# Kernel optimization log

Hardware: AMD Instinct MI355X
Metric: run time of the kernel (lower is better)

The kernel has to match this reference:

```python
import jax, jax.numpy as jnp
import numpy as np

B, N, C = 128, 196, 2048   # batch, regions (14x14), conv channels
H, A = 512, 512            # hidden_size, attention_size


def setup_inputs() -> dict:
    key = jax.random.key(0)
    ks = jax.random.split(key, 10)
    s = lambda d: 1.0 / np.sqrt(d)
    return {
        "img_embedding": jax.random.normal(ks[0], (B, N, C), jnp.float32),
        "hidden": jax.random.normal(ks[1], (B, H), jnp.float32),
        "W_img": jax.random.uniform(ks[2], (C, A), jnp.float32, -s(C), s(C)),
        "b_img": jax.random.uniform(ks[3], (A,), jnp.float32, -s(C), s(C)),
        "W_hid": jax.random.uniform(ks[4], (H, A), jnp.float32, -s(H), s(H)),
        "b_hid": jax.random.uniform(ks[5], (A,), jnp.float32, -s(H), s(H)),
        "w_att": jax.random.uniform(ks[6], (A,), jnp.float32, -s(A), s(A)),
        "b_att": jax.random.uniform(ks[7], (), jnp.float32, -s(A), s(A)),
        "w_beta": jax.random.uniform(ks[8], (H,), jnp.float32, -s(H), s(H)),
        "b_beta": jax.random.uniform(ks[9], (), jnp.float32, -s(H), s(H)),
    }


def reference(img_embedding, hidden, W_img, b_img, W_hid, b_hid,
              w_att, b_att, w_beta, b_beta):
    # img_embedding: (B, N, C); hidden: (B, H)
    img_att = jnp.einsum('bnc,ca->bna', img_embedding, W_img) + b_img   # (B,N,A)
    hid_att = hidden @ W_hid + b_hid                                    # (B,A)
    # additive attention scores -> (B, N)
    scores = jnp.einsum('bna,a->bn',
                        jax.nn.relu(img_att + hid_att[:, None, :]), w_att) + b_att
    beta = jax.nn.sigmoid(hidden @ w_beta + b_beta)                     # (B,)
    attention_weights = jax.nn.softmax(scores, axis=-1)                 # (B,N)
    context = beta[:, None] * jnp.einsum('bn,bnc->bc',
                                         attention_weights, img_embedding)  # (B,C)
    return context, attention_weights
```

## Files before the change

### kernel.cpp

```cpp
#include <hip/hip_runtime.h>
#include <hip/hip_bf16.h>
#include <math.h>

typedef __bf16 bf16v8 __attribute__((ext_vector_type(8)));
typedef float  f32x4  __attribute__((ext_vector_type(4)));

__device__ __forceinline__ void gload_lds16(const void* g, void* l) {
    __builtin_amdgcn_global_load_lds(
        (const __attribute__((address_space(1))) unsigned int*)g,
        (__attribute__((address_space(3))) unsigned int*)l, 16, 0, 0);
}

__device__ __forceinline__ void cvt_store8(void* dst, float4 a, float4 b) {
    bf16v8 v;
    v[0] = (__bf16)a.x; v[1] = (__bf16)a.y; v[2] = (__bf16)a.z; v[3] = (__bf16)a.w;
    v[4] = (__bf16)b.x; v[5] = (__bf16)b.y; v[6] = (__bf16)b.z; v[7] = (__bf16)b.w;
    *(bf16v8*)dst = v;
}

__global__ __launch_bounds__(256) void wt_k(const float* __restrict__ W,
                                            unsigned short* __restrict__ Wt)
{
    __shared__ float tile[64][65];
    const int k0 = blockIdx.x * 64;
    const int a0 = blockIdx.y * 64;
    const int t = threadIdx.x;
    const int c = t & 63, rbase = t >> 6;
#pragma unroll
    for (int i = 0; i < 16; ++i) {
        int kr = rbase + i * 4;
        tile[kr][c] = W[(k0 + kr) * 512 + a0 + c];
    }
    __syncthreads();
#pragma unroll
    for (int i = 0; i < 16; ++i) {
        int ar = rbase + i * 4;
        Wt[(a0 + ar) * 2048 + k0 + c] =
            __builtin_bit_cast(unsigned short, (__bf16)tile[c][ar]);
    }
}

__global__ __launch_bounds__(256) void hid_k(
    const float* __restrict__ hidden, const float* __restrict__ W_hid,
    const float* __restrict__ b_hid,  const float* __restrict__ b_img,
    const float* __restrict__ w_beta, const float* __restrict__ b_beta,
    float* __restrict__ hb, float* __restrict__ betap)
{
    const int b = blockIdx.x, t = threadIdx.x;
    __shared__ float hs[512];
    __shared__ float red[4];
    hs[t]       = hidden[b * 512 + t];
    hs[t + 256] = hidden[b * 512 + 256 + t];
    __syncthreads();
    float a0 = 0.f, a1 = 0.f;
#pragma unroll 4
    for (int h = 0; h < 512; ++h) {
        float hv = hs[h];
        a0 = fmaf(hv, W_hid[h * 512 + t], a0);
        a1 = fmaf(hv, W_hid[h * 512 + 256 + t], a1);
    }
    hb[b * 512 + t]       = a0 + b_hid[t]       + b_img[t];
    hb[b * 512 + 256 + t] = a1 + b_hid[256 + t] + b_img[256 + t];

    float x = hs[t] * w_beta[t] + hs[t + 256] * w_beta[t + 256];
#pragma unroll
    for (int k = 32; k >= 1; k >>= 1) x += __shfl_xor(x, k, 64);
    const int lane = t & 63, wid = t >> 6;
    if (lane == 0) red[wid] = x;
    __syncthreads();
    if (t == 0) {
        float s = red[0] + red[1] + red[2] + red[3] + b_beta[0];
        betap[b] = 1.f / (1.f + __expf(-s));
    }
}

__global__ __launch_bounds__(256, 3) void scores_gemm(
    const float* __restrict__ img,
    const unsigned short* __restrict__ Wt,
    const float* __restrict__ hb,
    const float* __restrict__ w_att,
    float* __restrict__ partials)
{
    __shared__ __align__(16) char smem[40960];
    char* A0 = smem;
    char* A1 = smem + 4096;
    char* B0 = smem + 8192;
    char* B1 = smem + 24576;

    const int tid  = threadIdx.x;
    const int lane = tid & 63;
    const int wid  = tid >> 6;

    const int id = blockIdx.x;
    const int wg = (id & 7) * 98 + (id >> 3);
    const int cb    = wg & 1;
    const int mtile = wg >> 1;
    const int r0 = mtile * 64;
    const int a0 = cb * 256;

    const int ar = tid >> 2;
    const int aq = tid & 3;
    const float* gA = img + (size_t)(r0 + ar) * 2048 + aq * 8;
    const int aW = ar * 64 + aq * 16;

    const int bswz = ((tid & 3) ^ ((tid >> 3) & 3)) * 8;
    const unsigned short* gBp0 = Wt + (size_t)(a0 + (tid >> 2)) * 2048 + bswz;
    const unsigned short* gBp1 = gBp0 + (size_t)64 * 2048;
    const unsigned short* gBp2 = gBp0 + (size_t)128 * 2048;
    const unsigned short* gBp3 = gBp0 + (size_t)192 * 2048;
    const int bW = tid * 16;

    const int g  = lane >> 4;
    const int fl = lane & 15;
    const int bro = (g ^ ((fl >> 1) & 3)) << 4;

    f32x4 acc[4][4] = {};
    float4 rA0[2], rA1[2];

#define ALOAD(RC, K) do {                                                    \
    RC[0] = *(const float4*)(gA + (K) * 32);                                 \
    RC[1] = *(const float4*)(gA + (K) * 32 + 4);                             \
} while (0)

#define STAGEB(K, NB) do {                                                   \
    gload_lds16(gBp0 + (K) * 32, NB + bW);                                   \
    gload_lds16(gBp1 + (K) * 32, NB + 4096 + bW);                            \
    gload_lds16(gBp2 + (K) * 32, NB + 8192 + bW);                            \
    gload_lds16(gBp3 + (K) * 32, NB + 12288 + bW);                           \
} while (0)

    ALOAD(rA0, 0);
    STAGEB(0, B0);
    __builtin_amdgcn_sched_barrier(0);
    cvt_store8(A0 + aW, rA0[0], rA0[1]);
    ALOAD(rA0, 1);
    ALOAD(rA1, 2);
    __syncthreads();

#define BODY(K, CA, CB, NA, NB, RC, STAGE, DOCVT, RELOAD, BAR) do {          \
    bf16v8 av[4], bv[4];                                                     \
    _Pragma("unroll")                                                        \
    for (int fm = 0; fm < 4; ++fm)                                           \
        av[fm] = *(const bf16v8*)(CA + (fm * 16 + fl) * 64 + g * 16);        \
    _Pragma("unroll")                                                        \
    for (int fn = 0; fn < 4; ++fn) {                                         \
        int col = wid * 64 + fn * 16 + fl;                                   \
        bv[fn] = *(const bf16v8*)(CB + col * 64 + bro);                      \
    }                                                                        \
    if (STAGE) STAGEB(K + 1, NB);                                            \
    __builtin_amdgcn_sched_barrier(0);                                       \
    if (DOCVT) cvt_store8(NA + aW, RC[0], RC[1]);                            \
    if (RELOAD) ALOAD(RC, K + 3);                                            \
    __builtin_amdgcn_sched_barrier(0);                                       \
    _Pragma("unroll")                                                        \
    for (int fm = 0; fm < 4; ++fm)                                           \
        _Pragma("unroll")                                                    \
        for (int fn = 0; fn < 4; ++fn)                                       \
            acc[fm][fn] = __builtin_amdgcn_mfma_f32_16x16x32_bf16(           \
                av[fm], bv[fn], acc[fm][fn], 0, 0, 0);                       \
    if (BAR == 1) {                                                          \
        __syncthreads();                                                     \
    } else if (BAR == 0) {                                                   \
        __builtin_amdgcn_sched_barrier(0);                                   \
        asm volatile("s_waitcnt vmcnt(2) lgkmcnt(0)" ::: "memory");          \
        __builtin_amdgcn_s_barrier();                                        \
        __builtin_amdgcn_sched_barrier(0);                                   \
    }                                                                        \
} while (0)

    for (int t = 0; t < 60; t += 2) {
        BODY(t,     A0, B0, A1, B1, rA0, true, true, true, 0);
        BODY(t + 1, A1, B1, A0, B0, rA1, true, true, true, 0);
    }
    BODY(60, A0, B0, A1, B1, rA0, true,  true,  true,  0);
    BODY(61, A1, B1, A0, B0, rA1, true,  true,  false, 1);
    BODY(62, A0, B0, A1, B1, rA0, true,  true,  false, 1);
    BODY(63, A1, B1, A0, B0, rA1, false, false, false, 2);
#undef BODY
#undef STAGEB
#undef ALOAD

    float* red = (float*)smem;
    const int l4 = lane >> 4;

    float w4[4];
#pragma unroll
    for (int fn = 0; fn < 4; ++fn) w4[fn] = w_att[a0 + wid * 64 + fn * 16 + fl];

#pragma unroll
    for (int fm = 0; fm < 4; ++fm) {
#pragma unroll
        for (int rg = 0; rg < 4; ++rg) {
            int row = fm * 16 + l4 * 4 + rg;
            int grow = r0 + row;
            int bb = grow / 196;
            const float* hbrow = hb + bb * 512 + a0 + wid * 64;
            float s = 0.f;
#pragma unroll
            for (int fn = 0; fn < 4; ++fn) {
                float v = acc[fm][fn][rg] + hbrow[fn * 16 + fl];
                v = fmaxf(v, 0.f);
                s = fmaf(v, w4[fn], s);
            }
#pragma unroll
            for (int m = 1; m < 16; m <<= 1) s += __shfl_xor(s, m, 64);
            if (fl == 0) red[wid * 64 + row] = s;
        }
    }
    __syncthreads();
    if (tid < 64) {
        partials[cb * 25088 + r0 + tid] =
            red[tid] + red[64 + tid] + red[128 + tid] + red[192 + tid];
    }
}

__global__ __launch_bounds__(256) void softmax_k(
    const float* __restrict__ partials, const float* __restrict__ betap,
    const float* __restrict__ b_att,
    float* __restrict__ out_w, float* __restrict__ wbeta)
{
    const int b = blockIdx.x;
    const int t = threadIdx.x;
    const int lane = t & 63, wid = t >> 6;
    __shared__ float red[4];

    float scv = 0.f, sc = -1e30f;
    if (t < 196) {
        int r = b * 196 + t;
        scv = partials[r] + partials[25088 + r] + b_att[0];
        sc = scv;
    }
    float m = sc;
#pragma unroll
    for (int k = 32; k >= 1; k >>= 1) m = fmaxf(m, __shfl_xor(m, k, 64));
    if (lane == 0) red[wid] = m;
    __syncthreads();
    m = fmaxf(fmaxf(red[0], red[1]), fmaxf(red[2], red[3]));

    float e = (t < 196) ? __expf(scv - m) : 0.f;
    float ssum = e;
#pragma unroll
    for (int k = 32; k >= 1; k >>= 1) ssum += __shfl_xor(ssum, k, 64);
    __syncthreads();
    if (lane == 0) red[wid] = ssum;
    __syncthreads();
    float denom = red[0] + red[1] + red[2] + red[3];

    if (t < 196) {
        float w = e / denom;
        out_w[b * 196 + t] = w;
        wbeta[b * 196 + t] = w * betap[b];
    }
}

__global__ __launch_bounds__(256) void ctx_k(
    const float* __restrict__ img, const float* __restrict__ wbeta,
    float* __restrict__ out)
{
    const int b = blockIdx.y;
    const int c0 = blockIdx.x * 512 + threadIdx.x * 2;
    __shared__ float w[200];
    if (threadIdx.x < 196) w[threadIdx.x] = wbeta[b * 196 + threadIdx.x];
    __syncthreads();
    const float* base = img + (size_t)b * 196 * 2048 + c0;
    float acx = 0.f, acy = 0.f;
#pragma unroll 4
    for (int n = 0; n < 196; ++n) {
        float2 v = *(const float2*)(base + (size_t)n * 2048);
        float wn = w[n];
        acx = fmaf(wn, v.x, acx);
        acy = fmaf(wn, v.y, acy);
    }
    float2 r; r.x = acx; r.y = acy;
    *(float2*)(out + b * 2048 + c0) = r;
}

extern "C" void kernel_launch(void* const* d_in, const int* in_sizes, int n_in,
                              void* d_out, int out_size, void* d_ws, size_t ws_size,
                              hipStream_t stream)
{
    const float* img    = (const float*)d_in[0];
    const float* hidden = (const float*)d_in[1];
    const float* W_img  = (const float*)d_in[2];
    const float* b_img  = (const float*)d_in[3];
    const float* W_hid  = (const float*)d_in[4];
    const float* b_hid  = (const float*)d_in[5];
    const float* w_att  = (const float*)d_in[6];
    const float* b_att  = (const float*)d_in[7];
    const float* w_beta = (const float*)d_in[8];
    const float* b_beta = (const float*)d_in[9];

    char* ws = (char*)d_ws;
    unsigned short* Wt = (unsigned short*)ws;
    float* hbp   = (float*)(ws + 2097152);
    float* betap = (float*)(ws + 2359296);
    float* parts = (float*)(ws + 2359808);
    float* wbeta = (float*)(ws + 2761216);

    float* out_ctx = (float*)d_out;
    float* out_w   = out_ctx + 128 * 2048;

    wt_k<<<dim3(32, 8), 256, 0, stream>>>(W_img, Wt);
    hid_k<<<128, 256, 0, stream>>>(hidden, W_hid, b_hid, b_img, w_beta, b_beta,
                                   hbp, betap);
    scores_gemm<<<784, 256, 0, stream>>>(img, Wt, hbp, w_att, parts);
    softmax_k<<<128, 256, 0, stream>>>(parts, betap, b_att, out_w, wbeta);
    ctx_k<<<dim3(4, 128), 256, 0, stream>>>(img, wbeta, out_ctx);
}
```

Before: 202.1 us.

## Pre-convert image embeddings to bf16 and use direct-to-LDS loads in scores GEMM

Adds a separate pass that converts the full fp32 image tensor to bf16 in workspace. The scores GEMM can then stream both operands with global-to-LDS loads into double-buffered tiles and feed bf16 MFMA without per-tile conversion. This aims to remove conversion work and register staging from the GEMM's inner loop. In exchange it adds an extra full read of the image tensor plus a write and re-read of a large bf16 copy, and it needs a much larger workspace, falling back to the old path otherwise.

```diff
diff --git a/kernel.cpp b/kernel.cpp
--- a/kernel.cpp
+++ b/kernel.cpp
@@ -16,6 +16,20 @@
     v[0] = (__bf16)a.x; v[1] = (__bf16)a.y; v[2] = (__bf16)a.z; v[3] = (__bf16)a.w;
     v[4] = (__bf16)b.x; v[5] = (__bf16)b.y; v[6] = (__bf16)b.z; v[7] = (__bf16)b.w;
     *(bf16v8*)dst = v;
+}
+
+__global__ __launch_bounds__(256) void cvt_k(const float* __restrict__ img,
+                                             unsigned short* __restrict__ imgb)
+{
+    const size_t nchunk = (size_t)25088 * 2048 / 8;
+    size_t i = (size_t)blockIdx.x * 256 + threadIdx.x;
+    const size_t stride = (size_t)gridDim.x * 256;
+    for (; i < nchunk; i += stride) {
+        const float* p = img + i * 8;
+        float4 a = *(const float4*)p;
+        float4 b = *(const float4*)(p + 4);
+        cvt_store8(imgb + i * 8, a, b);
+    }
 }
 
 __global__ __launch_bounds__(256) void wt_k(const float* __restrict__ W,
@@ -74,7 +88,109 @@
     }
 }
 
-__global__ __launch_bounds__(256, 3) void scores_gemm(
+__global__ __launch_bounds__(256, 3) void scores_m97(
+    const unsigned short* __restrict__ imgb,
+    const unsigned short* __restrict__ Wt,
+    const float* __restrict__ hb,
+    const float* __restrict__ w_att,
+    float* __restrict__ partials)
+{
+    __shared__ __align__(16) char smem[40960];
+    char* A0 = smem;
+    char* A1 = smem + 4096;
+    char* B0 = smem + 8192;
+    char* B1 = smem + 24576;
+
+    const int tid  = threadIdx.x;
+    const int lane = tid & 63;
+    const int wid  = tid >> 6;
+
+    const int id = blockIdx.x;
+    const int wg = (id & 7) * 98 + (id >> 3);
+    const int cb    = wg & 1;
+    const int mtile = wg >> 1;
+    const int r0 = mtile * 64;
+    const int a0 = cb * 256;
+
+    const unsigned short* gA = imgb + (size_t)(r0 + (tid >> 2)) * 2048 + (tid & 3) * 8;
+    const unsigned short* gB = Wt   + (size_t)(a0 + (tid >> 2)) * 2048 + (tid & 3) * 8;
+    const int dA = tid * 16;
+    const int dB = tid * 16;
+
+    const int g  = lane >> 4;
+    const int fl = lane & 15;
+
+    f32x4 acc[4][4] = {};
+
+#define STAGE(K, AB, BB) do {                                                \
+    gload_lds16(gA + (size_t)(K) * 32, AB + dA);                             \
+    gload_lds16(gB + (size_t)(K) * 32,                    BB + dB);          \
+    gload_lds16(gB + (size_t)64  * 2048 + (size_t)(K) * 32, BB + 4096  + dB);\
+    gload_lds16(gB + (size_t)128 * 2048 + (size_t)(K) * 32, BB + 8192  + dB);\
+    gload_lds16(gB + (size_t)192 * 2048 + (size_t)(K) * 32, BB + 12288 + dB);\
+} while (0)
+
+#define BODY(K, CA, CB, NA, NB) do {                                         \
+    if ((K) + 1 < 64) STAGE((K) + 1, NA, NB);                                \
+    bf16v8 av[4], bv[4];                                                     \
+    _Pragma("unroll")                                                        \
+    for (int fm = 0; fm < 4; ++fm)                                           \
+        av[fm] = *(const bf16v8*)(CA + (fm * 16 + fl) * 64 + g * 16);        \
+    _Pragma("unroll")                                                        \
+    for (int fn = 0; fn < 4; ++fn)                                           \
+        bv[fn] = *(const bf16v8*)(CB + (wid * 64 + fn * 16 + fl) * 64 + g * 16);\
+    _Pragma("unroll")                                                        \
+    for (int fm = 0; fm < 4; ++fm)                                           \
+        _Pragma("unroll")                                                    \
+        for (int fn = 0; fn < 4; ++fn)                                       \
+            acc[fm][fn] = __builtin_amdgcn_mfma_f32_16x16x32_bf16(           \
+                av[fm], bv[fn], acc[fm][fn], 0, 0, 0);                       \
+    __syncthreads();                                                         \
+} while (0)
+
+    STAGE(0, A0, B0);
+    __syncthreads();
+    for (int t = 0; t < 64; t += 2) {
+        BODY(t,     A0, B0, A1, B1);
+        BODY(t + 1, A1, B1, A0, B0);
+    }
+#undef BODY
+#undef STAGE
+
+    float* red = (float*)smem;
+
+    float w4[4];
+#pragma unroll
+    for (int fn = 0; fn < 4; ++fn) w4[fn] = w_att[a0 + wid * 64 + fn * 16 + fl];
+
+#pragma unroll
+    for (int fm = 0; fm < 4; ++fm) {
+#pragma unroll
+        for (int rg = 0; rg < 4; ++rg) {
+            int row = fm * 16 + g * 4 + rg;
+            int grow = r0 + row;
+            int bb = grow / 196;
+            const float* hbrow = hb + bb * 512 + a0 + wid * 64;
+            float s = 0.f;
+#pragma unroll
+            for (int fn = 0; fn < 4; ++fn) {
+                float v = acc[fm][fn][rg] + hbrow[fn * 16 + fl];
+                v = fmaxf(v, 0.f);
+                s = fmaf(v, w4[fn], s);
+            }
+#pragma unroll
+            for (int m = 1; m < 16; m <<= 1) s += __shfl_xor(s, m, 64);
+            if (fl == 0) red[wid * 64 + row] = s;
+        }
+    }
+    __syncthreads();
+    if (tid < 64) {
+        partials[cb * 25088 + r0 + tid] =
+            red[tid] + red[64 + tid] + red[128 + tid] + red[192 + tid];
+    }
+}
+
+__global__ __launch_bounds__(256, 3) void scores_fb(
     const float* __restrict__ img,
     const unsigned short* __restrict__ Wt,
     const float* __restrict__ hb,
@@ -290,20 +406,41 @@
     const float* w_beta = (const float*)d_in[8];
     const float* b_beta = (const float*)d_in[9];
 
-    char* ws = (char*)d_ws;
-    unsigned short* Wt = (unsigned short*)ws;
-    float* hbp   = (float*)(ws + 2097152);
-    float* betap = (float*)(ws + 2359296);
-    float* parts = (float*)(ws + 2359808);
-    float* wbeta = (float*)(ws + 2761216);
-
     float* out_ctx = (float*)d_out;
     float* out_w   = out_ctx + 128 * 2048;
 
-    wt_k<<<dim3(32, 8), 256, 0, stream>>>(W_img, Wt);
-    hid_k<<<128, 256, 0, stream>>>(hidden, W_hid, b_hid, b_img, w_beta, b_beta,
-                                   hbp, betap);
-    scores_gemm<<<784, 256, 0, stream>>>(img, Wt, hbp, w_att, parts);
-    softmax_k<<<128, 256, 0, stream>>>(parts, betap, b_att, out_w, wbeta);
-    ctx_k<<<dim3(4, 128), 256, 0, stream>>>(img, wbeta, out_ctx);
-}
+    char* ws = (char*)d_ws;
+    const size_t IMGB_BYTES = (size_t)25088 * 2048 * 2;
+    const size_t NEED = IMGB_BYTES + 2097152 + 262144 + 512 + 200704 + 100352;
+
+    if (ws_size >= NEED) {
+        unsigned short* imgb = (unsigned short*)ws;
+        char* ws2 = ws + IMGB_BYTES;
+        unsigned short* Wt = (unsigned short*)ws2;
+        float* hbp   = (float*)(ws2 + 2097152);
+        float* betap = (float*)(ws2 + 2097152 + 262144);
+        float* parts = (float*)(ws2 + 2097152 + 262144 + 512);
+        float* wbeta = (float*)(ws2 + 2097152 + 262144 + 512 + 200704);
+
+        cvt_k<<<4096, 256, 0, stream>>>(img, imgb);
+        wt_k<<<dim3(32, 8), 256, 0, stream>>>(W_img, Wt);
+        hid_k<<<128, 256, 0, stream>>>(hidden, W_hid, b_hid, b_img,
+                                       w_beta, b_beta, hbp, betap);
+        scores_m97<<<784, 256, 0, stream>>>(imgb, Wt, hbp, w_att, parts);
+        softmax_k<<<128, 256, 0, stream>>>(parts, betap, b_att, out_w, wbeta);
+        ctx_k<<<dim3(4, 128), 256, 0, stream>>>(img, wbeta, out_ctx);
+    } else {
+        unsigned short* Wt = (unsigned short*)ws;
+        float* hbp   = (float*)(ws + 2097152);
+        float* betap = (float*)(ws + 2359296);
+        float* parts = (float*)(ws + 2359808);
+        float* wbeta = (float*)(ws + 2761216);
+
+        wt_k<<<dim3(32, 8), 256, 0, stream>>>(W_img, Wt);
+        hid_k<<<128, 256, 0, stream>>>(hidden, W_hid, b_hid, b_img,
+                                       w_beta, b_beta, hbp, betap);
+        scores_fb<<<784, 256, 0, stream>>>(img, Wt, hbp, w_att, parts);
+        softmax_k<<<128, 256, 0, stream>>>(parts, betap, b_att, out_w, wbeta);
+        ctx_k<<<dim3(4, 128), 256, 0, stream>>>(img, wbeta, out_ctx);
+    }
+}
```

Measured after the change: 253.3 us. 25.3% more time.
